# Performance work log

Measured on AMD Instinct MI355X. Metric: run time of the kernel, lower is better.

The kernel has to match this reference:

```python
import jax, jax.numpy as jnp
import numpy as np


def setup_inputs() -> dict:
    key = jax.random.key(0)
    k1, k2 = jax.random.split(key)
    bs, L, H, C = 4, 512, 768, 48
    hidden_states = jax.random.normal(k1, (bs, L, H), dtype=jnp.float32)
    # xavier_uniform for Linear(2H -> C): bound = sqrt(6/(2H+C))
    bound = float(np.sqrt(6.0 / (2 * H + C)))
    W = jax.random.uniform(k2, (C, 2 * H), dtype=jnp.float32, minval=-bound, maxval=bound)
    b = jnp.zeros((C,), dtype=jnp.float32)
    return {"hidden_states": hidden_states, "W": W, "b": b}


def reference(hidden_states, W, b):
    # hidden_states: (bs, L, H); W: (C, 2H); b: (C,)
    # Original: logits[b,i,j,:] = W @ concat(h_i, h_j) + b (dropout in eval = identity).
    # Split W = [W_i | W_j] along input dim -> two small projections + broadcast sum,
    # avoiding the O(L^2 * 2H) pair tensor.
    H = hidden_states.shape[-1]
    W_i, W_j = W[:, :H], W[:, H:]
    proj_i = jnp.einsum("blh,ch->blc", hidden_states, W_i)  # (bs, L, C)
    proj_j = jnp.einsum("blh,ch->blc", hidden_states, W_j)  # (bs, L, C)
    logits = proj_i[:, :, None, :] + proj_j[:, None, :, :] + b  # (bs, L, L, C)
    return logits
```

## Files before the change

### kernel.cpp

```cpp
#include <hip/hip_runtime.h>

typedef float f32x4 __attribute__((ext_vector_type(4)));

#define H_DIM 768
#define C_DIM 48
#define NROWS 2048
#define TWO_H 1536

#define BM 64
#define BK 32
#define KSLICE 96
#define NSTEP (KSLICE / BK)
#define KS 8
#define LDA 36
#define LDB 36
#define PART_ELEMS (KS * NROWS * 96)

__global__ __launch_bounds__(256) void pgemm_kernel(const float* __restrict__ hs,
                                                    const float* __restrict__ W,
                                                    float* __restrict__ part) {
    __shared__ float A_lds[2][BM][LDA];
    __shared__ float B_lds[2][96][LDB];

    const int t     = threadIdx.x;
    const int kg    = blockIdx.x & 7;
    const int rg    = blockIdx.x >> 3;
    const int row0  = rg * BM;
    const int kbase = kg * KSLICE;

    const int r4 = t >> 4;
    const int c6 = t & 15;

    const f32x4* __restrict__ hs4 = reinterpret_cast<const f32x4*>(hs);

    const int a_row = t >> 3;
    const int a_kf4 = t & 7;

    f32x4 a_reg[2], b_reg[3];

    {
        const int k0 = kbase;
        #pragma unroll
        for (int i = 0; i < 2; ++i)
            a_reg[i] = hs4[(size_t)(row0 + a_row + i * 32) * (H_DIM / 4) + (k0 >> 2) + a_kf4];
        #pragma unroll
        for (int q = 0; q < 3; ++q) {
            const int idx  = q * 256 + t;
            const int c    = idx >> 3;
            const int kf4  = idx & 7;
            const int half = c / C_DIM;
            const int cc   = c - half * C_DIM;
            b_reg[q] = *reinterpret_cast<const f32x4*>(
                W + (size_t)cc * TWO_H + (size_t)half * H_DIM + k0 + kf4 * 4);
        }
    }
    {
        #pragma unroll
        for (int i = 0; i < 2; ++i)
            *reinterpret_cast<f32x4*>(&A_lds[0][a_row + i * 32][a_kf4 * 4]) = a_reg[i];
        #pragma unroll
        for (int q = 0; q < 3; ++q) {
            const int idx = q * 256 + t;
            const int c   = idx >> 3;
            const int kf4 = idx & 7;
            *reinterpret_cast<f32x4*>(&B_lds[0][c][kf4 * 4]) = b_reg[q];
        }
    }

    float acc[4][6];
    #pragma unroll
    for (int ri = 0; ri < 4; ++ri)
        #pragma unroll
        for (int j = 0; j < 6; ++j) acc[ri][j] = 0.f;

    for (int s = 0; s < NSTEP; ++s) {
        __syncthreads();

        if (s + 1 < NSTEP) {
            const int k0 = kbase + (s + 1) * BK;
            #pragma unroll
            for (int i = 0; i < 2; ++i)
                a_reg[i] = hs4[(size_t)(row0 + a_row + i * 32) * (H_DIM / 4) + (k0 >> 2) + a_kf4];
            #pragma unroll
            for (int q = 0; q < 3; ++q) {
                const int idx  = q * 256 + t;
                const int c    = idx >> 3;
                const int kf4  = idx & 7;
                const int half = c / C_DIM;
                const int cc   = c - half * C_DIM;
                b_reg[q] = *reinterpret_cast<const f32x4*>(
                    W + (size_t)cc * TWO_H + (size_t)half * H_DIM + k0 + kf4 * 4);
            }
        }

        const int buf = s & 1;
        #pragma unroll
        for (int kk4 = 0; kk4 < BK / 4; ++kk4) {
            f32x4 a[4], b[6];
            #pragma unroll
            for (int ri = 0; ri < 4; ++ri)
                a[ri] = *reinterpret_cast<const f32x4*>(&A_lds[buf][r4 * 4 + ri][kk4 * 4]);
            #pragma unroll
            for (int j = 0; j < 6; ++j)
                b[j] = *reinterpret_cast<const f32x4*>(&B_lds[buf][c6 + j * 16][kk4 * 4]);
            #pragma unroll
            for (int ri = 0; ri < 4; ++ri)
                #pragma unroll
                for (int j = 0; j < 6; ++j) {
                    acc[ri][j] += a[ri].x * b[j].x;
                    acc[ri][j] += a[ri].y * b[j].y;
                    acc[ri][j] += a[ri].z * b[j].z;
                    acc[ri][j] += a[ri].w * b[j].w;
                }
        }

        __syncthreads();

        if (s + 1 < NSTEP) {
            const int buf2 = (s + 1) & 1;
            #pragma unroll
            for (int i = 0; i < 2; ++i)
                *reinterpret_cast<f32x4*>(&A_lds[buf2][a_row + i * 32][a_kf4 * 4]) = a_reg[i];
            #pragma unroll
            for (int q = 0; q < 3; ++q) {
                const int idx = q * 256 + t;
                const int c   = idx >> 3;
                const int kf4 = idx & 7;
                *reinterpret_cast<f32x4*>(&B_lds[buf2][c][kf4 * 4]) = b_reg[q];
            }
        }
    }

    float* __restrict__ pslab = part + (size_t)kg * (NROWS * 96);
    #pragma unroll
    for (int ri = 0; ri < 4; ++ri) {
        const int row = row0 + r4 * 4 + ri;
        #pragma unroll
        for (int j = 0; j < 6; ++j)
            pslab[(size_t)row * 96 + c6 + j * 16] = acc[ri][j];
    }
}

__global__ __launch_bounds__(256) void preduce_kernel(const float* __restrict__ part,
                                                      float* __restrict__ proj) {
    const int p = blockIdx.x * 256 + threadIdx.x;
    const f32x4* __restrict__ part4 = reinterpret_cast<const f32x4*>(part);

    f32x4 v = part4[p];
    #pragma unroll
    for (int g = 1; g < 8; ++g)
        v += part4[(size_t)g * (NROWS * 24) + p];

    const int row  = p / 24;
    const int c4   = p % 24;
    const int half = c4 / 12;
    const int cl4  = c4 % 12;
    reinterpret_cast<f32x4*>(proj)[(size_t)half * (NROWS * 12) + (size_t)row * 12 + cl4] = v;
}

__global__ __launch_bounds__(256) void bcast_kernel(const float* __restrict__ proj,
                                                    const float* __restrict__ bias,
                                                    float* __restrict__ out) {
    const int gi = blockIdx.x;
    const int b  = gi >> 9;

    __shared__ f32x4 rowi[C_DIM / 4];

    const int t = threadIdx.x;
    if (t < C_DIM / 4) {
        f32x4 pi = reinterpret_cast<const f32x4*>(proj + (size_t)gi * C_DIM)[t];
        f32x4 bb = reinterpret_cast<const f32x4*>(bias)[t];
        rowi[t] = pi + bb;
    }
    __syncthreads();

    const f32x4* __restrict__ pj =
        reinterpret_cast<const f32x4*>(proj + (size_t)NROWS * C_DIM
                                            + (size_t)b * 512 * C_DIM);
    f32x4* __restrict__ o =
        reinterpret_cast<f32x4*>(out) + (size_t)gi * 6144;

    #pragma unroll
    for (int it = 0; it < 24; ++it) {
        const int p  = it * 256 + t;
        o[p] = pj[p] + rowi[p % 12];
    }
}

extern "C" void kernel_launch(void* const* d_in, const int* in_sizes, int n_in,
                              void* d_out, int out_size, void* d_ws, size_t ws_size,
                              hipStream_t stream) {
    const float* hs   = (const float*)d_in[0];
    const float* W    = (const float*)d_in[1];
    const float* bias = (const float*)d_in[2];
    float* out  = (float*)d_out;
    float* proj = (float*)d_ws;

    float* part = out + (size_t)out_size - PART_ELEMS;

    pgemm_kernel<<<dim3(256), 256, 0, stream>>>(hs, W, part);
    preduce_kernel<<<dim3(192), 256, 0, stream>>>(part, proj);
    bcast_kernel<<<dim3(NROWS), 256, 0, stream>>>(proj, bias, out);
}
```

Measured before the change: 49.12 us.

## Replace split-K GEMM plus reduce with full-K GEMM and in-block reduction

Drops the 8-way split-K projection GEMM, which wrote partial slabs into the output buffer, and the separate reduction kernel. Each block now covers 16 rows and one half of W over the full K range. Its two thread groups each take half of every K tile and are combined through shared memory before the block writes proj directly. This saves one kernel launch and the partial-sum traffic, but each block runs a longer serial K loop with less work per thread.

```diff
diff --git a/kernel.cpp b/kernel.cpp
--- a/kernel.cpp
+++ b/kernel.cpp
@@ -7,106 +7,115 @@
 #define NROWS 2048
 #define TWO_H 1536
 
-#define BM 64
-#define BK 32
-#define KSLICE 96
-#define NSTEP (KSLICE / BK)
-#define KS 8
-#define LDA 36
-#define LDB 36
-#define PART_ELEMS (KS * NROWS * 96)
-
-__global__ __launch_bounds__(256) void pgemm_kernel(const float* __restrict__ hs,
-                                                    const float* __restrict__ W,
-                                                    float* __restrict__ part) {
-    __shared__ float A_lds[2][BM][LDA];
-    __shared__ float B_lds[2][96][LDB];
-
-    const int t     = threadIdx.x;
-    const int kg    = blockIdx.x & 7;
-    const int rg    = blockIdx.x >> 3;
-    const int row0  = rg * BM;
-    const int kbase = kg * KSLICE;
-
-    const int r4 = t >> 4;
-    const int c6 = t & 15;
+#define GBM 16
+#define GBK 128
+#define GNSTEP (H_DIM / GBK)
+#define GLDA 132
+#define GLDB 132
+#define MT_LD 52
+
+__global__ __launch_bounds__(256) void gemm_kernel(const float* __restrict__ hs,
+                                                   const float* __restrict__ W,
+                                                   float* __restrict__ proj) {
+    __shared__ float A_lds[2][GBM][GLDA];
+    __shared__ float B_lds[2][C_DIM][GLDB];
+    __shared__ float mtile[GBM][MT_LD];
+
+    const int t    = threadIdx.x;
+    const int half = blockIdx.x & 1;
+    const int rg   = blockIdx.x >> 1;
+    const int row0 = rg * GBM;
+
+    const int kgrp = t >> 7;
+    const int tt   = t & 127;
+    const int rs   = tt >> 4;
+    const int cs   = tt & 15;
 
     const f32x4* __restrict__ hs4 = reinterpret_cast<const f32x4*>(hs);
-
-    const int a_row = t >> 3;
-    const int a_kf4 = t & 7;
-
-    f32x4 a_reg[2], b_reg[3];
+    const float* __restrict__ Wh  = W + (size_t)half * H_DIM;
+
+    f32x4 a_reg[2], b_reg[6];
 
     {
-        const int k0 = kbase;
-        #pragma unroll
-        for (int i = 0; i < 2; ++i)
-            a_reg[i] = hs4[(size_t)(row0 + a_row + i * 32) * (H_DIM / 4) + (k0 >> 2) + a_kf4];
-        #pragma unroll
-        for (int q = 0; q < 3; ++q) {
-            const int idx  = q * 256 + t;
-            const int c    = idx >> 3;
-            const int kf4  = idx & 7;
-            const int half = c / C_DIM;
-            const int cc   = c - half * C_DIM;
+        const int k0 = 0;
+        #pragma unroll
+        for (int q = 0; q < 2; ++q) {
+            const int idx = q * 256 + t;
+            const int row = idx >> 5;
+            const int kf4 = idx & 31;
+            a_reg[q] = hs4[(size_t)(row0 + row) * (H_DIM / 4) + (k0 >> 2) + kf4];
+        }
+        #pragma unroll
+        for (int q = 0; q < 6; ++q) {
+            const int idx = q * 256 + t;
+            const int c   = idx >> 5;
+            const int kf4 = idx & 31;
             b_reg[q] = *reinterpret_cast<const f32x4*>(
-                W + (size_t)cc * TWO_H + (size_t)half * H_DIM + k0 + kf4 * 4);
+                Wh + (size_t)c * TWO_H + k0 + kf4 * 4);
         }
     }
     {
         #pragma unroll
-        for (int i = 0; i < 2; ++i)
-            *reinterpret_cast<f32x4*>(&A_lds[0][a_row + i * 32][a_kf4 * 4]) = a_reg[i];
-        #pragma unroll
-        for (int q = 0; q < 3; ++q) {
-            const int idx = q * 256 + t;
-            const int c   = idx >> 3;
-            const int kf4 = idx & 7;
+        for (int q = 0; q < 2; ++q) {
+            const int idx = q * 256 + t;
+            const int row = idx >> 5;
+            const int kf4 = idx & 31;
+            *reinterpret_cast<f32x4*>(&A_lds[0][row][kf4 * 4]) = a_reg[q];
+        }
+        #pragma unroll
+        for (int q = 0; q < 6; ++q) {
+            const int idx = q * 256 + t;
+            const int c   = idx >> 5;
+            const int kf4 = idx & 31;
             *reinterpret_cast<f32x4*>(&B_lds[0][c][kf4 * 4]) = b_reg[q];
         }
     }
 
-    float acc[4][6];
+    float acc[2][3];
     #pragma unroll
-    for (int ri = 0; ri < 4; ++ri)
-        #pragma unroll
-        for (int j = 0; j < 6; ++j) acc[ri][j] = 0.f;
-
-    for (int s = 0; s < NSTEP; ++s) {
+    for (int ri = 0; ri < 2; ++ri)
+        #pragma unroll
+        for (int j = 0; j < 3; ++j) acc[ri][j] = 0.f;
+
+    const int kb4 = kgrp * 16;
+
+    for (int s = 0; s < GNSTEP; ++s) {
         __syncthreads();
 
-        if (s + 1 < NSTEP) {
-            const int k0 = kbase + (s + 1) * BK;
-            #pragma unroll
-            for (int i = 0; i < 2; ++i)
-                a_reg[i] = hs4[(size_t)(row0 + a_row + i * 32) * (H_DIM / 4) + (k0 >> 2) + a_kf4];
-            #pragma unroll
-            for (int q = 0; q < 3; ++q) {
-                const int idx  = q * 256 + t;
-                const int c    = idx >> 3;
-                const int kf4  = idx & 7;
-                const int half = c / C_DIM;
-                const int cc   = c - half * C_DIM;
+        if (s + 1 < GNSTEP) {
+            const int k0 = (s + 1) * GBK;
+            #pragma unroll
+            for (int q = 0; q < 2; ++q) {
+                const int idx = q * 256 + t;
+                const int row = idx >> 5;
+                const int kf4 = idx & 31;
+                a_reg[q] = hs4[(size_t)(row0 + row) * (H_DIM / 4) + (k0 >> 2) + kf4];
+            }
+            #pragma unroll
+            for (int q = 0; q < 6; ++q) {
+                const int idx = q * 256 + t;
+                const int c   = idx >> 5;
+                const int kf4 = idx & 31;
                 b_reg[q] = *reinterpret_cast<const f32x4*>(
-                    W + (size_t)cc * TWO_H + (size_t)half * H_DIM + k0 + kf4 * 4);
+                    Wh + (size_t)c * TWO_H + k0 + kf4 * 4);
             }
         }
 
         const int buf = s & 1;
         #pragma unroll
-        for (int kk4 = 0; kk4 < BK / 4; ++kk4) {
-            f32x4 a[4], b[6];
-            #pragma unroll
-            for (int ri = 0; ri < 4; ++ri)
-                a[ri] = *reinterpret_cast<const f32x4*>(&A_lds[buf][r4 * 4 + ri][kk4 * 4]);
-            #pragma unroll
-            for (int j = 0; j < 6; ++j)
-                b[j] = *reinterpret_cast<const f32x4*>(&B_lds[buf][c6 + j * 16][kk4 * 4]);
-            #pragma unroll
-            for (int ri = 0; ri < 4; ++ri)
+        for (int kk4 = 0; kk4 < GBK / 4 / 2; ++kk4) {
+            const int kz = (kb4 + kk4) * 4;
+            f32x4 a[2], b[3];
+            #pragma unroll
+            for (int ri = 0; ri < 2; ++ri)
+                a[ri] = *reinterpret_cast<const f32x4*>(&A_lds[buf][rs * 2 + ri][kz]);
+            #pragma unroll
+            for (int j = 0; j < 3; ++j)
+                b[j] = *reinterpret_cast<const f32x4*>(&B_lds[buf][cs * 3 + j][kz]);
+            #pragma unroll
+            for (int ri = 0; ri < 2; ++ri)
                 #pragma unroll
-                for (int j = 0; j < 6; ++j) {
+                for (int j = 0; j < 3; ++j) {
                     acc[ri][j] += a[ri].x * b[j].x;
                     acc[ri][j] += a[ri].y * b[j].y;
                     acc[ri][j] += a[ri].z * b[j].z;
@@ -116,46 +125,50 @@
 
         __syncthreads();
 
-        if (s + 1 < NSTEP) {
+        if (s + 1 < GNSTEP) {
             const int buf2 = (s + 1) & 1;
             #pragma unroll
-            for (int i = 0; i < 2; ++i)
-                *reinterpret_cast<f32x4*>(&A_lds[buf2][a_row + i * 32][a_kf4 * 4]) = a_reg[i];
-            #pragma unroll
-            for (int q = 0; q < 3; ++q) {
-                const int idx = q * 256 + t;
-                const int c   = idx >> 3;
-                const int kf4 = idx & 7;
+            for (int q = 0; q < 2; ++q) {
+                const int idx = q * 256 + t;
+                const int row = idx >> 5;
+                const int kf4 = idx & 31;
+                *reinterpret_cast<f32x4*>(&A_lds[buf2][row][kf4 * 4]) = a_reg[q];
+            }
+            #pragma unroll
+            for (int q = 0; q < 6; ++q) {
+                const int idx = q * 256 + t;
+                const int c   = idx >> 5;
+                const int kf4 = idx & 31;
                 *reinterpret_cast<f32x4*>(&B_lds[buf2][c][kf4 * 4]) = b_reg[q];
             }
         }
     }
 
-    float* __restrict__ pslab = part + (size_t)kg * (NROWS * 96);
-    #pragma unroll
-    for (int ri = 0; ri < 4; ++ri) {
-        const int row = row0 + r4 * 4 + ri;
-        #pragma unroll
-        for (int j = 0; j < 6; ++j)
-            pslab[(size_t)row * 96 + c6 + j * 16] = acc[ri][j];
-    }
-}
-
-__global__ __launch_bounds__(256) void preduce_kernel(const float* __restrict__ part,
-                                                      float* __restrict__ proj) {
-    const int p = blockIdx.x * 256 + threadIdx.x;
-    const f32x4* __restrict__ part4 = reinterpret_cast<const f32x4*>(part);
-
-    f32x4 v = part4[p];
-    #pragma unroll
-    for (int g = 1; g < 8; ++g)
-        v += part4[(size_t)g * (NROWS * 24) + p];
-
-    const int row  = p / 24;
-    const int c4   = p % 24;
-    const int half = c4 / 12;
-    const int cl4  = c4 % 12;
-    reinterpret_cast<f32x4*>(proj)[(size_t)half * (NROWS * 12) + (size_t)row * 12 + cl4] = v;
+    __syncthreads();
+    if (kgrp == 1) {
+        #pragma unroll
+        for (int ri = 0; ri < 2; ++ri)
+            #pragma unroll
+            for (int j = 0; j < 3; ++j)
+                mtile[rs * 2 + ri][cs * 3 + j] = acc[ri][j];
+    }
+    __syncthreads();
+    if (kgrp == 0) {
+        #pragma unroll
+        for (int ri = 0; ri < 2; ++ri)
+            #pragma unroll
+            for (int j = 0; j < 3; ++j)
+                mtile[rs * 2 + ri][cs * 3 + j] += acc[ri][j];
+    }
+    __syncthreads();
+
+    if (t < GBM * 12) {
+        const int row = t / 12;
+        const int c4  = t % 12;
+        const f32x4 v = *reinterpret_cast<const f32x4*>(&mtile[row][c4 * 4]);
+        reinterpret_cast<f32x4*>(proj)[(size_t)half * (NROWS * 12)
+                                       + (size_t)(row0 + row) * 12 + c4] = v;
+    }
 }
 
 __global__ __launch_bounds__(256) void bcast_kernel(const float* __restrict__ proj,
@@ -196,9 +209,6 @@
     float* out  = (float*)d_out;
     float* proj = (float*)d_ws;
 
-    float* part = out + (size_t)out_size - PART_ELEMS;
-
-    pgemm_kernel<<<dim3(256), 256, 0, stream>>>(hs, W, part);
-    preduce_kernel<<<dim3(192), 256, 0, stream>>>(part, proj);
+    gemm_kernel<<<dim3(256), 256, 0, stream>>>(hs, W, proj);
     bcast_kernel<<<dim3(NROWS), 256, 0, stream>>>(proj, bias, out);
 }
```

New measurement: 47.77 us. 2.7% less time.
